# Kernel tuning notes

Hardware: AMD Instinct MI355X
Metric: run time of the kernel (lower is better)

Reference implementation:

```python
import jax, jax.numpy as jnp
import numpy as np

TEMP = 0.5   # cosine-similarity temperature divisor
EPS = 1e-8   # torch F.cosine_similarity norm clamp


def setup_inputs() -> dict:
    key = jax.random.key(0)
    k1, k2, k3 = jax.random.split(key, 3)
    N, C, L, K = 8, 256, 512, 100
    z = jax.random.normal(k1, (N, C, L), dtype=jnp.float32)        # encoder features
    c = jax.random.normal(k2, (N, C, L + 1), dtype=jnp.float32)    # transformer out (start token)
    neg_inds = jax.random.randint(k3, (N, L, K), 0, N * L)          # flat indices into (N*L, C)
    return {"z": z, "c": c, "neg_inds": neg_inds}


def _normalize(x):
    return x / jnp.maximum(jnp.linalg.norm(x, axis=-1, keepdims=True), EPS)


def reference(z, c, neg_inds):
    N, C, L = z.shape
    K = neg_inds.shape[-1]

    # sample_negatives: gather distractors from flattened (N*L, C) features
    z_seq = jnp.transpose(z, (0, 2, 1))                 # (N, L, C)
    z_flat = z_seq.reshape(-1, C)                        # (N*L, C)
    negatives = z_flat[neg_inds.reshape(-1)].reshape(N, L, K, C)

    # compute_logits: cosine similarity of context vs [positive, negatives]
    c_seq = jnp.transpose(c[..., 1:], (0, 2, 1))         # (N, L, C), drop start token
    cn = _normalize(c_seq)
    zn = _normalize(z_seq)
    nn = _normalize(negatives)

    pos_logit = jnp.sum(cn * zn, axis=-1)                # (N, L)
    neg_logits = jnp.einsum('nlc,nlkc->nlk', cn, nn)     # (N, L, K)

    # mask negatives that exactly equal the context vector
    neg_in_target = jnp.all(c_seq[:, :, None, :] == negatives, axis=-1)  # (N, L, K)
    neg_logits = jnp.where(neg_in_target, -jnp.inf, neg_logits)

    logits = jnp.concatenate([pos_logit[..., None], neg_logits], axis=-1) / TEMP
    logits = logits.reshape(-1, K + 1)                   # (N*L, K+1)

    # contrastive_loss: cross-entropy with target class 0 (the positive)
    loss = jnp.mean(jax.nn.logsumexp(logits, axis=-1) - logits[:, 0])
    return loss
```

## Files before the change

### kernel.cpp

```cpp
#include <hip/hip_runtime.h>
#include <math.h>

#define N 8
#define C 256
#define L 512
#define K 100
#define NL (N * L)
#define EPSN 1e-8f


__device__ __forceinline__ unsigned short f2bf_rne(float x) {
    unsigned u = __float_as_uint(x);
    u += 0x7fffu + ((u >> 16) & 1u);
    return (unsigned short)(u >> 16);
}
__device__ __forceinline__ float bf_lo(unsigned d) { return __uint_as_float(d << 16); }
__device__ __forceinline__ float bf_hi(unsigned d) { return __uint_as_float(d & 0xffff0000u); }

__global__ __launch_bounds__(256) void prep_kernel(
    const float* __restrict__ z, const float* __restrict__ c,
    unsigned short* __restrict__ znb, unsigned short* __restrict__ cnb)
{
    __shared__ float tile[256 * 33];
    __shared__ float red[256];
    __shared__ float linv[32];

    const int b    = blockIdx.x;
    const int is_c = b >= 128;
    const int bb   = b & 127;
    const int n    = bb >> 4;
    const int l0   = (bb & 15) << 5;
    const int ld   = is_c ? (L + 1) : L;
    const float* src = (is_c ? c : z) + (size_t)n * C * ld + (is_c ? 1 : 0) + l0;
    unsigned short* dst = (is_c ? cnb : znb) + (size_t)(n * L + l0) * C;

    const int t   = threadIdx.x;
    const int lcl = t & 31;
    const int cg  = t >> 5;

    float ss = 0.f;
    #pragma unroll
    for (int i = 0; i < 32; ++i) {
        const int cidx = i * 8 + cg;
        const float v = src[(size_t)cidx * ld + lcl];
        tile[cidx * 33 + lcl] = v;
        ss += v * v;
    }
    red[t] = ss;
    __syncthreads();
    if (t < 32) {
        float tot = 0.f;
        #pragma unroll
        for (int j = 0; j < 8; ++j) tot += red[j * 32 + t];
        linv[t] = 1.f / fmaxf(sqrtf(tot), EPSN);
    }
    __syncthreads();
    #pragma unroll
    for (int j = 0; j < 32; ++j)
        dst[(size_t)j * C + t] = f2bf_rne(tile[t * 33 + j] * linv[j]);
}

__global__ __launch_bounds__(256) void logits_kernel(
    const unsigned short* __restrict__ znb, const unsigned short* __restrict__ cnb,
    const int* __restrict__ neg,
    const float* __restrict__ z, const float* __restrict__ c,
    float* __restrict__ partials)
{
    __shared__ float buf[4][2 * 16 * 68];
    __shared__ float wterm[4];

    const int w    = threadIdx.x >> 6;
    const int lane = threadIdx.x & 63;
    const int row  = __builtin_amdgcn_readfirstlane((int)blockIdx.x * 4 + w);
    const int* __restrict__ negp = neg + (size_t)row * K;
    float* __restrict__ bw = &buf[w][0];

    const int h = lane >> 5;
    const int k = lane & 31;

    const uint4 cd = *(const uint4*)(cnb + (size_t)row * C + k * 8);
    const float c0 = bf_lo(cd.x), c1 = bf_hi(cd.x);
    const float c2 = bf_lo(cd.y), c3 = bf_hi(cd.y);
    const float c4 = bf_lo(cd.z), c5 = bf_hi(cd.z);
    const float c6 = bf_lo(cd.w), c7 = bf_hi(cd.w);

    float s_acc = 0.f, pos = 0.f;

    #pragma unroll 2
    for (int b = 0; b < 4; ++b) {
        float* __restrict__ pb = bw + (b & 1) * (16 * 68);
        #pragma unroll
        for (int r = 0; r < 16; ++r) {
            const int t0 = b * 32 + 2 * r;
            const int i0 = (t0 == 0) ? row :
                ((t0 <= K) ? __builtin_amdgcn_readfirstlane(negp[t0 - 1]) : row);
            const int i1 = (t0 + 1 <= K) ?
                __builtin_amdgcn_readfirstlane(negp[t0]) : row;
            const int idx = h ? i1 : i0;
            const uint4 zd = *(const uint4*)(znb + (size_t)idx * C + k * 8);
            const float p =
                fmaf(c0, bf_lo(zd.x), fmaf(c1, bf_hi(zd.x),
                fmaf(c2, bf_lo(zd.y), fmaf(c3, bf_hi(zd.y),
                fmaf(c4, bf_lo(zd.z), fmaf(c5, bf_hi(zd.z),
                fmaf(c6, bf_lo(zd.w), c7 * bf_hi(zd.w))))))));
            pb[r * 68 + h * 32 + k] = p;
        }
        const int tt = lane & 31, hl = lane >> 5;
        const int rr = tt >> 1, hh = tt & 1;
        const float* q = pb + rr * 68 + hh * 32 + hl * 16;
        const float4 a0 = *(const float4*)(q);
        const float4 a1 = *(const float4*)(q + 4);
        const float4 a2 = *(const float4*)(q + 8);
        const float4 a3 = *(const float4*)(q + 12);
        float d = ((a0.x + a0.y) + (a0.z + a0.w))
                + ((a1.x + a1.y) + (a1.z + a1.w))
                + ((a2.x + a2.y) + (a2.z + a2.w))
                + ((a3.x + a3.y) + (a3.z + a3.w));
        d += __shfl_xor(d, 32, 64);

        const int t = b * 32 + tt;
        const float sim2 = d * 2.0f;
        if (t == 0 && hl == 0) pos = sim2;

        bool use = (hl == 0) && (t <= K);
        if (use && t >= 1 && sim2 > 1.9f) {
            const int idxv = negp[t - 1];
            const int nr = row >> 9, lr = row & 511;
            const int ni = idxv >> 9, li = idxv & 511;
            bool eq = true;
            for (int e = 0; e < C && eq; ++e)
                eq = (c[((size_t)nr * C + e) * (L + 1) + lr + 1]
                      == z[((size_t)ni * C + e) * L + li]);
            if (eq) use = false;
        }
        if (use) s_acc += __expf(sim2 - 2.0f);
    }

    #pragma unroll
    for (int m = 1; m < 64; m <<= 1) s_acc += __shfl_xor(s_acc, m, 64);
    if (lane == 0) wterm[w] = 2.0f + __logf(s_acc) - pos;
    __syncthreads();
    if (threadIdx.x == 0)
        partials[blockIdx.x] = wterm[0] + wterm[1] + wterm[2] + wterm[3];
}

__global__ __launch_bounds__(256) void reduce_kernel(
    const float* __restrict__ p, float* __restrict__ out)
{
    __shared__ float red[4];
    const int t = threadIdx.x;
    float s = p[t] + p[t + 256] + p[t + 512] + p[t + 768];
    #pragma unroll
    for (int m = 1; m < 64; m <<= 1) s += __shfl_xor(s, m, 64);
    if ((t & 63) == 0) red[t >> 6] = s;
    __syncthreads();
    if (t == 0) out[0] = (red[0] + red[1] + red[2] + red[3]) * (1.0f / NL);
}

extern "C" void kernel_launch(void* const* d_in, const int* in_sizes, int n_in,
                              void* d_out, int out_size, void* d_ws, size_t ws_size,
                              hipStream_t stream) {
    const float* z = (const float*)d_in[0];
    const float* c = (const float*)d_in[1];
    const int* neg = (const int*)d_in[2];
    float* out = (float*)d_out;

    unsigned short* znb = (unsigned short*)d_ws;
    unsigned short* cnb = znb + (size_t)NL * C;
    float* partials = (float*)(cnb + (size_t)NL * C);

    prep_kernel<<<256, 256, 0, stream>>>(z, c, znb, cnb);
    logits_kernel<<<NL / 4, 256, 0, stream>>>(znb, cnb, neg, z, c, partials);
    reduce_kernel<<<1, 256, 0, stream>>>(partials, out);
}
```

Measured before the change: 83.68 us.

## Store normalized z as FP8 and keep context vectors in fp32

```diff
diff --git a/kernel.cpp b/kernel.cpp
--- a/kernel.cpp
+++ b/kernel.cpp
@@ -9,17 +9,15 @@
 #define EPSN 1e-8f
 
 
-__device__ __forceinline__ unsigned short f2bf_rne(float x) {
-    unsigned u = __float_as_uint(x);
-    u += 0x7fffu + ((u >> 16) & 1u);
-    return (unsigned short)(u >> 16);
+typedef float v2f __attribute__((ext_vector_type(2)));
+
+__device__ __forceinline__ unsigned char f2fp8(float x) {
+    return (unsigned char)(__builtin_amdgcn_cvt_pk_fp8_f32(x, x, 0, false) & 0xff);
 }
-__device__ __forceinline__ float bf_lo(unsigned d) { return __uint_as_float(d << 16); }
-__device__ __forceinline__ float bf_hi(unsigned d) { return __uint_as_float(d & 0xffff0000u); }
 
 __global__ __launch_bounds__(256) void prep_kernel(
     const float* __restrict__ z, const float* __restrict__ c,
-    unsigned short* __restrict__ znb, unsigned short* __restrict__ cnb)
+    unsigned char* __restrict__ zq, float* __restrict__ cn)
 {
     __shared__ float tile[256 * 33];
     __shared__ float red[256];
@@ -32,7 +30,6 @@
     const int l0   = (bb & 15) << 5;
     const int ld   = is_c ? (L + 1) : L;
     const float* src = (is_c ? c : z) + (size_t)n * C * ld + (is_c ? 1 : 0) + l0;
-    unsigned short* dst = (is_c ? cnb : znb) + (size_t)(n * L + l0) * C;
 
     const int t   = threadIdx.x;
     const int lcl = t & 31;
@@ -55,13 +52,21 @@
         linv[t] = 1.f / fmaxf(sqrtf(tot), EPSN);
     }
     __syncthreads();
-    #pragma unroll
-    for (int j = 0; j < 32; ++j)
-        dst[(size_t)j * C + t] = f2bf_rne(tile[t * 33 + j] * linv[j]);
+    if (is_c) {
+        float* dst = cn + (size_t)(n * L + l0) * C;
+        #pragma unroll
+        for (int j = 0; j < 32; ++j)
+            dst[(size_t)j * C + t] = tile[t * 33 + j] * linv[j];
+    } else {
+        unsigned char* dst = zq + (size_t)(n * L + l0) * C;
+        #pragma unroll
+        for (int j = 0; j < 32; ++j)
+            dst[(size_t)j * C + t] = f2fp8(tile[t * 33 + j] * linv[j]);
+    }
 }
 
-__global__ __launch_bounds__(256) void logits_kernel(
-    const unsigned short* __restrict__ znb, const unsigned short* __restrict__ cnb,
+__global__ __launch_bounds__(256, 4) void logits_kernel(
+    const unsigned char* __restrict__ zq, const float* __restrict__ cn,
     const int* __restrict__ neg,
     const float* __restrict__ z, const float* __restrict__ c,
     float* __restrict__ partials)
@@ -69,60 +74,67 @@
     __shared__ float buf[4][2 * 16 * 68];
     __shared__ float wterm[4];
 
-    const int w    = threadIdx.x >> 6;
-    const int lane = threadIdx.x & 63;
-    const int row  = __builtin_amdgcn_readfirstlane((int)blockIdx.x * 4 + w);
+    const int w = threadIdx.x >> 6, lane = threadIdx.x & 63;
+    const int row = __builtin_amdgcn_readfirstlane((int)blockIdx.x * 4 + w);
     const int* __restrict__ negp = neg + (size_t)row * K;
-    float* __restrict__ bw = &buf[w][0];
+    const int g = lane >> 4;
+    const int k = lane & 15;
 
-    const int h = lane >> 5;
-    const int k = lane & 31;
-
-    const uint4 cd = *(const uint4*)(cnb + (size_t)row * C + k * 8);
-    const float c0 = bf_lo(cd.x), c1 = bf_hi(cd.x);
-    const float c2 = bf_lo(cd.y), c3 = bf_hi(cd.y);
-    const float c4 = bf_lo(cd.z), c5 = bf_hi(cd.z);
-    const float c6 = bf_lo(cd.w), c7 = bf_hi(cd.w);
+    const float* crow = cn + (size_t)row * C + k * 16;
+    const float4 ca = *(const float4*)(crow);
+    const float4 cb = *(const float4*)(crow + 4);
+    const float4 cc = *(const float4*)(crow + 8);
+    const float4 ce = *(const float4*)(crow + 12);
 
     float s_acc = 0.f, pos = 0.f;
 
-    #pragma unroll 2
-    for (int b = 0; b < 4; ++b) {
-        float* __restrict__ pb = bw + (b & 1) * (16 * 68);
-        #pragma unroll
+    #pragma unroll 1
+    for (int b = 0; b < 2; ++b) {
+        float* __restrict__ pb = &buf[w][b * (16 * 68)];
+        #pragma unroll 8
         for (int r = 0; r < 16; ++r) {
-            const int t0 = b * 32 + 2 * r;
-            const int i0 = (t0 == 0) ? row :
-                ((t0 <= K) ? __builtin_amdgcn_readfirstlane(negp[t0 - 1]) : row);
-            const int i1 = (t0 + 1 <= K) ?
-                __builtin_amdgcn_readfirstlane(negp[t0]) : row;
-            const int idx = h ? i1 : i0;
-            const uint4 zd = *(const uint4*)(znb + (size_t)idx * C + k * 8);
-            const float p =
-                fmaf(c0, bf_lo(zd.x), fmaf(c1, bf_hi(zd.x),
-                fmaf(c2, bf_lo(zd.y), fmaf(c3, bf_hi(zd.y),
-                fmaf(c4, bf_lo(zd.z), fmaf(c5, bf_hi(zd.z),
-                fmaf(c6, bf_lo(zd.w), c7 * bf_hi(zd.w))))))));
-            pb[r * 68 + h * 32 + k] = p;
+            const int t0 = b * 64 + 4 * r;
+            const int i0 = (t0 == 0) ? row
+                : ((t0 <= K) ? __builtin_amdgcn_readfirstlane(negp[t0 - 1]) : row);
+            const int i1 = (t0 + 1 <= K) ? __builtin_amdgcn_readfirstlane(negp[t0]) : row;
+            const int i2 = (t0 + 2 <= K) ? __builtin_amdgcn_readfirstlane(negp[t0 + 1]) : row;
+            const int i3 = (t0 + 3 <= K) ? __builtin_amdgcn_readfirstlane(negp[t0 + 2]) : row;
+            const int idx = (g == 0) ? i0 : (g == 1) ? i1 : (g == 2) ? i2 : i3;
+            const uint4 zd = *(const uint4*)(zq + (size_t)idx * C + k * 16);
+            v2f q;
+            float d;
+            q = __builtin_amdgcn_cvt_pk_f32_fp8(zd.x, false);
+            d = ca.x * q.x; d = fmaf(ca.y, q.y, d);
+            q = __builtin_amdgcn_cvt_pk_f32_fp8(zd.x, true);
+            d = fmaf(ca.z, q.x, d); d = fmaf(ca.w, q.y, d);
+            q = __builtin_amdgcn_cvt_pk_f32_fp8(zd.y, false);
+            d = fmaf(cb.x, q.x, d); d = fmaf(cb.y, q.y, d);
+            q = __builtin_amdgcn_cvt_pk_f32_fp8(zd.y, true);
+            d = fmaf(cb.z, q.x, d); d = fmaf(cb.w, q.y, d);
+            q = __builtin_amdgcn_cvt_pk_f32_fp8(zd.z, false);
+            d = fmaf(cc.x, q.x, d); d = fmaf(cc.y, q.y, d);
+            q = __builtin_amdgcn_cvt_pk_f32_fp8(zd.z, true);
+            d = fmaf(cc.z, q.x, d); d = fmaf(cc.w, q.y, d);
+            q = __builtin_amdgcn_cvt_pk_f32_fp8(zd.w, false);
+            d = fmaf(ce.x, q.x, d); d = fmaf(ce.y, q.y, d);
+            q = __builtin_amdgcn_cvt_pk_f32_fp8(zd.w, true);
+            d = fmaf(ce.z, q.x, d); d = fmaf(ce.w, q.y, d);
+            pb[r * 68 + g * 16 + k] = d;
         }
-        const int tt = lane & 31, hl = lane >> 5;
-        const int rr = tt >> 1, hh = tt & 1;
-        const float* q = pb + rr * 68 + hh * 32 + hl * 16;
-        const float4 a0 = *(const float4*)(q);
-        const float4 a1 = *(const float4*)(q + 4);
-        const float4 a2 = *(const float4*)(q + 8);
-        const float4 a3 = *(const float4*)(q + 12);
-        float d = ((a0.x + a0.y) + (a0.z + a0.w))
-                + ((a1.x + a1.y) + (a1.z + a1.w))
-                + ((a2.x + a2.y) + (a2.z + a2.w))
-                + ((a3.x + a3.y) + (a3.z + a3.w));
-        d += __shfl_xor(d, 32, 64);
+        const int t = b * 64 + lane;
+        const float* qp = pb + (lane >> 2) * 68 + (lane & 3) * 16;
+        const float4 a0 = *(const float4*)(qp);
+        const float4 a1 = *(const float4*)(qp + 4);
+        const float4 a2 = *(const float4*)(qp + 8);
+        const float4 a3 = *(const float4*)(qp + 12);
+        const float dt = ((a0.x + a0.y) + (a0.z + a0.w))
+                       + ((a1.x + a1.y) + (a1.z + a1.w))
+                       + ((a2.x + a2.y) + (a2.z + a2.w))
+                       + ((a3.x + a3.y) + (a3.z + a3.w));
+        const float sim2 = dt * 2.0f;
+        if (t == 0) pos = sim2;
 
-        const int t = b * 32 + tt;
-        const float sim2 = d * 2.0f;
-        if (t == 0 && hl == 0) pos = sim2;
-
-        bool use = (hl == 0) && (t <= K);
+        bool use = (t <= K);
         if (use && t >= 1 && sim2 > 1.9f) {
             const int idxv = negp[t - 1];
             const int nr = row >> 9, lr = row & 511;
@@ -165,11 +177,11 @@
     const int* neg = (const int*)d_in[2];
     float* out = (float*)d_out;
 
-    unsigned short* znb = (unsigned short*)d_ws;
-    unsigned short* cnb = znb + (size_t)NL * C;
-    float* partials = (float*)(cnb + (size_t)NL * C);
+    float* cn = (float*)d_ws;
+    unsigned char* zq = (unsigned char*)(cn + (size_t)NL * C);
+    float* partials = (float*)(zq + (size_t)NL * C);
 
-    prep_kernel<<<256, 256, 0, stream>>>(z, c, znb, cnb);
-    logits_kernel<<<NL / 4, 256, 0, stream>>>(znb, cnb, neg, z, c, partials);
+    prep_kernel<<<256, 256, 0, stream>>>(z, c, zq, cn);
+    logits_kernel<<<NL / 4, 256, 0, stream>>>(zq, cn, neg, z, c, partials);
     reduce_kernel<<<1, 256, 0, stream>>>(partials, out);
 }
```

New measurement: 82.34 us. Within noise of the previous version (-1.6%).
